# Kernel optimization log

Measured on AMD Instinct MI355X. Metric: run time of the kernel, lower is better.

## Reference

```python
import jax, jax.numpy as jnp
import numpy as np

B, L, D = 32, 4096, 1024


def setup_inputs() -> dict:
    key = jax.random.key(0)
    k_h, k_idx, k_w1, k_w2 = jax.random.split(key, 4)
    h = jax.random.normal(k_h, (B, L, D), dtype=jnp.float32)
    # 4 sorted positions per sample: [s1, e1, s2, e2]; +arange*2 guarantees
    # strict increase and a non-empty context region (s2 > e1 + 1).
    raw = jnp.sort(jax.random.randint(k_idx, (B, 4), 0, L - 10), axis=-1)
    pts = raw + jnp.arange(4, dtype=raw.dtype) * 2
    span1_idx = pts[:, 0:2].reshape(B, 1, 2).astype(jnp.int64)
    span2_idx = pts[:, 2:4].reshape(B, 1, 2).astype(jnp.int64)
    scale1 = 1.0 / np.sqrt(3 * D)
    scale2 = 1.0 / np.sqrt(D)
    W1 = jax.random.normal(k_w1, (3 * D, D), dtype=jnp.float32) * scale1
    b1 = jnp.zeros((D,), dtype=jnp.float32)
    W2 = jax.random.normal(k_w2, (D, D), dtype=jnp.float32) * scale2
    b2 = jnp.zeros((D,), dtype=jnp.float32)
    return {"h": h, "span1_idx": span1_idx, "span2_idx": span2_idx,
            "W1": W1, "b1": b1, "W2": W2, "b2": b2}


def _masked_mean(h, lo, hi_excl):
    # mean of h[b, lo[b]:hi_excl[b], :] over the length axis, vectorized
    pos = jnp.arange(h.shape[1])  # [L]
    mask = ((pos[None, :] >= lo[:, None]) & (pos[None, :] < hi_excl[:, None])).astype(h.dtype)  # [B,L]
    cnt = jnp.maximum(mask.sum(axis=1, keepdims=True), 1.0)  # [B,1]
    return jnp.einsum('bl,bld->bd', mask, h) / cnt  # [B,D]


def reference(h, span1_idx, span2_idx, W1, b1, W2, b2):
    s1, e1 = span1_idx[:, 0, 0], span1_idx[:, 0, 1]
    s2, e2 = span2_idx[:, 0, 0], span2_idx[:, 0, 1]
    span1_rep = _masked_mean(h, s1, e1 + 1)          # span tokens inclusive
    span2_rep = _masked_mean(h, s2, e2 + 1)
    context_rep = _masked_mean(h, e1 + 1, s2)        # tokens strictly between spans
    combined = jnp.concatenate([span1_rep, context_rep, span2_rep], axis=-1)  # [B,3D]
    hmid = jax.nn.relu(combined @ W1 + b1)
    out = hmid @ W2 + b2
    return out[:, None, :]  # [B,1,D]
```

## Files before the change

### kernel.cpp

```cpp
#include <hip/hip_runtime.h>

#define BB 32
#define LL 4096
#define DD 1024
#define G1 2048
#define K2_TILE 32
#define K3_TILE 16

static __device__ __forceinline__ int imax(int a, int b) { return a > b ? a : b; }
static __device__ __forceinline__ int imin(int a, int b) { return a < b ? a : b; }

__global__ __launch_bounds__(256) void k0_zero(float* __restrict__ sums_hmid,
                                               float* __restrict__ out) {
    const int i = blockIdx.x * 256 + threadIdx.x;
    const float4 z = make_float4(0.f, 0.f, 0.f, 0.f);
    if (i < 32768) ((float4*)sums_hmid)[i] = z;
    else ((float4*)out)[i - 32768] = z;
}

static __device__ __forceinline__ void accum_rows_add(const float* __restrict__ hb,
                                                      int beg, int end, float4& acc) {
    float4 a0 = make_float4(0.f, 0.f, 0.f, 0.f);
    float4 a1 = a0, a2 = a0, a3 = a0, a4 = a0, a5 = a0, a6 = a0, a7 = a0;
    int l = beg;
    for (; l + 8 <= end; l += 8) {
        float4 v0 = *(const float4*)(hb + (size_t)(l + 0) * DD);
        float4 v1 = *(const float4*)(hb + (size_t)(l + 1) * DD);
        float4 v2 = *(const float4*)(hb + (size_t)(l + 2) * DD);
        float4 v3 = *(const float4*)(hb + (size_t)(l + 3) * DD);
        float4 v4 = *(const float4*)(hb + (size_t)(l + 4) * DD);
        float4 v5 = *(const float4*)(hb + (size_t)(l + 5) * DD);
        float4 v6 = *(const float4*)(hb + (size_t)(l + 6) * DD);
        float4 v7 = *(const float4*)(hb + (size_t)(l + 7) * DD);
        a0.x += v0.x; a0.y += v0.y; a0.z += v0.z; a0.w += v0.w;
        a1.x += v1.x; a1.y += v1.y; a1.z += v1.z; a1.w += v1.w;
        a2.x += v2.x; a2.y += v2.y; a2.z += v2.z; a2.w += v2.w;
        a3.x += v3.x; a3.y += v3.y; a3.z += v3.z; a3.w += v3.w;
        a4.x += v4.x; a4.y += v4.y; a4.z += v4.z; a4.w += v4.w;
        a5.x += v5.x; a5.y += v5.y; a5.z += v5.z; a5.w += v5.w;
        a6.x += v6.x; a6.y += v6.y; a6.z += v6.z; a6.w += v6.w;
        a7.x += v7.x; a7.y += v7.y; a7.z += v7.z; a7.w += v7.w;
    }
    for (; l + 4 <= end; l += 4) {
        float4 v0 = *(const float4*)(hb + (size_t)(l + 0) * DD);
        float4 v1 = *(const float4*)(hb + (size_t)(l + 1) * DD);
        float4 v2 = *(const float4*)(hb + (size_t)(l + 2) * DD);
        float4 v3 = *(const float4*)(hb + (size_t)(l + 3) * DD);
        a0.x += v0.x; a0.y += v0.y; a0.z += v0.z; a0.w += v0.w;
        a1.x += v1.x; a1.y += v1.y; a1.z += v1.z; a1.w += v1.w;
        a2.x += v2.x; a2.y += v2.y; a2.z += v2.z; a2.w += v2.w;
        a3.x += v3.x; a3.y += v3.y; a3.z += v3.z; a3.w += v3.w;
    }
    for (; l < end; ++l) {
        float4 v = *(const float4*)(hb + (size_t)l * DD);
        a0.x += v.x; a0.y += v.y; a0.z += v.z; a0.w += v.w;
    }
    acc.x += ((a0.x + a1.x) + (a2.x + a3.x)) + ((a4.x + a5.x) + (a6.x + a7.x));
    acc.y += ((a0.y + a1.y) + (a2.y + a3.y)) + ((a4.y + a5.y) + (a6.y + a7.y));
    acc.z += ((a0.z + a1.z) + (a2.z + a3.z)) + ((a4.z + a5.z) + (a6.z + a7.z));
    acc.w += ((a0.w + a1.w) + (a2.w + a3.w)) + ((a4.w + a5.w) + (a6.w + a7.w));
}

__global__ __launch_bounds__(256) void k1_sums(const float* __restrict__ h,
                                               const int* __restrict__ sp1,
                                               const int* __restrict__ sp2,
                                               float* __restrict__ sums) {
    const int tid = threadIdx.x;

    int NC = 0;
#pragma unroll
    for (int b = 0; b < BB; ++b)
        NC += sp2[2 * b + 1] - sp1[2 * b] + 1;

    const int q = NC / G1, r = NC % G1;
    const int bk = blockIdx.x;
    int c0 = bk * q + imin(bk, r);
    const int c1 = c0 + q + (bk < r ? 1 : 0);
    if (c0 >= c1) return;

    int b = 0, base = 0, s1, e1, s2, e2, len;
    for (;; ++b) {
        s1 = sp1[2 * b]; e1 = sp1[2 * b + 1];
        s2 = sp2[2 * b]; e2 = sp2[2 * b + 1];
        len = e2 - s1 + 1;
        if (c0 < base + len) break;
        base += len;
    }

    for (;;) {
        const int cend = imin(c1, base + len);
        const int rb = s1 + (c0 - base);
        const int re = s1 + (cend - base);
        const float* hb = h + (size_t)b * LL * DD + (size_t)tid * 4;
        float* dstb = sums + (size_t)b * 3 * DD + (size_t)tid * 4;
        const int lo[3] = {rb, imax(rb, e1 + 1), imax(rb, s2)};
        const int hi[3] = {imin(re, e1 + 1), imin(re, s2), re};
#pragma unroll
        for (int s = 0; s < 3; ++s) {
            if (lo[s] < hi[s]) {
                float4 acc = make_float4(0.f, 0.f, 0.f, 0.f);
                accum_rows_add(hb, lo[s], hi[s], acc);
                float* d = dstb + s * DD;
                atomicAdd(d + 0, acc.x); atomicAdd(d + 1, acc.y);
                atomicAdd(d + 2, acc.z); atomicAdd(d + 3, acc.w);
            }
        }
        c0 = cend;
        if (c0 >= c1) break;
        base += len; ++b;
        s1 = sp1[2 * b]; e1 = sp1[2 * b + 1];
        s2 = sp2[2 * b]; e2 = sp2[2 * b + 1];
        len = e2 - s1 + 1;
    }
}

__global__ __launch_bounds__(256) void k2_gemm1(const float* __restrict__ sums,
                                                const int* __restrict__ sp1,
                                                const int* __restrict__ sp2,
                                                const float* __restrict__ W1,
                                                float* __restrict__ hmid) {
    __shared__ float cl[K2_TILE * BB];
    __shared__ float icl[BB];
    const int tid = threadIdx.x;
    const int j = blockIdx.x * 256 + tid;
    const int k0 = blockIdx.y * K2_TILE;
    const int seg = k0 / DD;

    if (tid < BB) {
        const int b = tid;
        const int s1 = sp1[2 * b], e1 = sp1[2 * b + 1];
        const int s2 = sp2[2 * b], e2 = sp2[2 * b + 1];
        const int cnt = (seg == 0) ? (e1 + 1 - s1) : (seg == 1) ? (s2 - e1 - 1) : (e2 + 1 - s2);
        icl[b] = 1.0f / (float)imax(cnt, 1);
    }
    __syncthreads();
    for (int i = tid; i < K2_TILE * BB; i += 256) {
        const int kk = i / BB;
        const int b = i % BB;
        cl[i] = sums[(size_t)b * (3 * DD) + (k0 + kk)] * icl[b];
    }
    __syncthreads();

    float acc[BB];
#pragma unroll
    for (int b = 0; b < BB; ++b) acc[b] = 0.f;

    const float* w = W1 + (size_t)k0 * DD + j;
#pragma unroll 8
    for (int kk = 0; kk < K2_TILE; ++kk) {
        const float wv = w[(size_t)kk * DD];
        const float4* c4 = (const float4*)(cl + kk * BB);
#pragma unroll
        for (int qq = 0; qq < BB / 4; ++qq) {
            float4 c = c4[qq];
            acc[4 * qq + 0] = fmaf(c.x, wv, acc[4 * qq + 0]);
            acc[4 * qq + 1] = fmaf(c.y, wv, acc[4 * qq + 1]);
            acc[4 * qq + 2] = fmaf(c.z, wv, acc[4 * qq + 2]);
            acc[4 * qq + 3] = fmaf(c.w, wv, acc[4 * qq + 3]);
        }
    }
#pragma unroll
    for (int b = 0; b < BB; ++b) atomicAdd(&hmid[(size_t)b * DD + j], acc[b]);
}

__global__ __launch_bounds__(256) void k3_gemm2(const float* __restrict__ hmid,
                                                const float* __restrict__ b1,
                                                const float* __restrict__ W2,
                                                const float* __restrict__ b2,
                                                float* __restrict__ out) {
    __shared__ float al[K3_TILE * BB];
    const int tid = threadIdx.x;
    const int j = blockIdx.x * 256 + tid;
    const int k0 = blockIdx.y * K3_TILE;

    for (int i = tid; i < K3_TILE * BB; i += 256) {
        const int kk = i / BB;
        const int b = i % BB;
        const float v = hmid[(size_t)b * DD + (k0 + kk)] + b1[k0 + kk];
        al[i] = fmaxf(v, 0.f);
    }
    __syncthreads();

    float acc[BB];
    const float bias = (blockIdx.y == 0) ? b2[j] : 0.f;
#pragma unroll
    for (int b = 0; b < BB; ++b) acc[b] = bias;

    const float* w = W2 + (size_t)k0 * DD + j;
#pragma unroll 8
    for (int kk = 0; kk < K3_TILE; ++kk) {
        const float wv = w[(size_t)kk * DD];
        const float4* c4 = (const float4*)(al + kk * BB);
#pragma unroll
        for (int qq = 0; qq < BB / 4; ++qq) {
            float4 c = c4[qq];
            acc[4 * qq + 0] = fmaf(c.x, wv, acc[4 * qq + 0]);
            acc[4 * qq + 1] = fmaf(c.y, wv, acc[4 * qq + 1]);
            acc[4 * qq + 2] = fmaf(c.z, wv, acc[4 * qq + 2]);
            acc[4 * qq + 3] = fmaf(c.w, wv, acc[4 * qq + 3]);
        }
    }
#pragma unroll
    for (int b = 0; b < BB; ++b) atomicAdd(&out[(size_t)b * DD + j], acc[b]);
}

extern "C" void kernel_launch(void* const* d_in, const int* in_sizes, int n_in,
                              void* d_out, int out_size, void* d_ws, size_t ws_size,
                              hipStream_t stream) {
    const float* h = (const float*)d_in[0];
    const int* sp1 = (const int*)d_in[1];
    const int* sp2 = (const int*)d_in[2];
    const float* W1 = (const float*)d_in[3];
    const float* b1 = (const float*)d_in[4];
    const float* W2 = (const float*)d_in[5];
    const float* b2 = (const float*)d_in[6];
    float* out = (float*)d_out;

    float* sums = (float*)d_ws;
    float* hmid = sums + BB * 3 * DD;

    k0_zero<<<160, 256, 0, stream>>>((float*)d_ws, out);
    k1_sums<<<G1, 256, 0, stream>>>(h, sp1, sp2, sums);
    k2_gemm1<<<dim3(DD / 256, 3 * DD / K2_TILE), 256, 0, stream>>>(sums, sp1, sp2, W1, hmid);
    k3_gemm2<<<dim3(DD / 256, DD / K3_TILE), 256, 0, stream>>>(hmid, b1, W2, b2, out);
}
```

Before: 111.9 us.

## Fuse span-sum and two GEMM kernels into one persistent kernel with grid barriers

The three separate launches (span sums, first GEMM, second GEMM) become one persistent kernel of 768 blocks. Phases are separated by software grid barriers built on atomic counters and flags in the workspace, and the zero kernel now also clears those barrier words. The goal is to drop launch gaps and tail effects between stages. In exchange the span-sum phase has fewer blocks (768 vs 2048) with a shallower unroll, and the barriers rely on every block being co-resident, which risks a deadlock if occupancy falls short.

```diff
diff --git a/kernel.cpp b/kernel.cpp
--- a/kernel.cpp
+++ b/kernel.cpp
@@ -3,44 +3,46 @@
 #define BB 32
 #define LL 4096
 #define DD 1024
-#define G1 2048
-#define K2_TILE 32
-#define K3_TILE 16
+#define GRID 768
+#define K2T 32
+#define K3T 16
 
 static __device__ __forceinline__ int imax(int a, int b) { return a > b ? a : b; }
 static __device__ __forceinline__ int imin(int a, int b) { return a < b ? a : b; }
 
-__global__ __launch_bounds__(256) void k0_zero(float* __restrict__ sums_hmid,
+#define BAR_OFF 131072
+
+__global__ __launch_bounds__(256) void k0_zero(float* __restrict__ ws,
                                                float* __restrict__ out) {
     const int i = blockIdx.x * 256 + threadIdx.x;
     const float4 z = make_float4(0.f, 0.f, 0.f, 0.f);
-    if (i < 32768) ((float4*)sums_hmid)[i] = z;
-    else ((float4*)out)[i - 32768] = z;
+    if (i < 32832) ((float4*)ws)[i] = z;
+    else if (i < 32832 + 8192) ((float4*)out)[i - 32832] = z;
+}
+
+static __device__ __forceinline__ void gbar(unsigned* cnt, unsigned* flag, int nb) {
+    __syncthreads();
+    if (threadIdx.x == 0) {
+        __threadfence();
+        const unsigned old = __hip_atomic_fetch_add(cnt, 1u, __ATOMIC_ACQ_REL,
+                                                    __HIP_MEMORY_SCOPE_AGENT);
+        if ((int)old == nb - 1) {
+            __hip_atomic_store(flag, 1u, __ATOMIC_RELEASE, __HIP_MEMORY_SCOPE_AGENT);
+        } else {
+            while (__hip_atomic_load(flag, __ATOMIC_ACQUIRE,
+                                     __HIP_MEMORY_SCOPE_AGENT) == 0u)
+                __builtin_amdgcn_s_sleep(1);
+        }
+        __threadfence();
+    }
+    __syncthreads();
 }
 
 static __device__ __forceinline__ void accum_rows_add(const float* __restrict__ hb,
                                                       int beg, int end, float4& acc) {
     float4 a0 = make_float4(0.f, 0.f, 0.f, 0.f);
-    float4 a1 = a0, a2 = a0, a3 = a0, a4 = a0, a5 = a0, a6 = a0, a7 = a0;
+    float4 a1 = a0, a2 = a0, a3 = a0;
     int l = beg;
-    for (; l + 8 <= end; l += 8) {
-        float4 v0 = *(const float4*)(hb + (size_t)(l + 0) * DD);
-        float4 v1 = *(const float4*)(hb + (size_t)(l + 1) * DD);
-        float4 v2 = *(const float4*)(hb + (size_t)(l + 2) * DD);
-        float4 v3 = *(const float4*)(hb + (size_t)(l + 3) * DD);
-        float4 v4 = *(const float4*)(hb + (size_t)(l + 4) * DD);
-        float4 v5 = *(const float4*)(hb + (size_t)(l + 5) * DD);
-        float4 v6 = *(const float4*)(hb + (size_t)(l + 6) * DD);
-        float4 v7 = *(const float4*)(hb + (size_t)(l + 7) * DD);
-        a0.x += v0.x; a0.y += v0.y; a0.z += v0.z; a0.w += v0.w;
-        a1.x += v1.x; a1.y += v1.y; a1.z += v1.z; a1.w += v1.w;
-        a2.x += v2.x; a2.y += v2.y; a2.z += v2.z; a2.w += v2.w;
-        a3.x += v3.x; a3.y += v3.y; a3.z += v3.z; a3.w += v3.w;
-        a4.x += v4.x; a4.y += v4.y; a4.z += v4.z; a4.w += v4.w;
-        a5.x += v5.x; a5.y += v5.y; a5.z += v5.z; a5.w += v5.w;
-        a6.x += v6.x; a6.y += v6.y; a6.z += v6.z; a6.w += v6.w;
-        a7.x += v7.x; a7.y += v7.y; a7.z += v7.z; a7.w += v7.w;
-    }
     for (; l + 4 <= end; l += 4) {
         float4 v0 = *(const float4*)(hb + (size_t)(l + 0) * DD);
         float4 v1 = *(const float4*)(hb + (size_t)(l + 1) * DD);
@@ -55,153 +57,159 @@
         float4 v = *(const float4*)(hb + (size_t)l * DD);
         a0.x += v.x; a0.y += v.y; a0.z += v.z; a0.w += v.w;
     }
-    acc.x += ((a0.x + a1.x) + (a2.x + a3.x)) + ((a4.x + a5.x) + (a6.x + a7.x));
-    acc.y += ((a0.y + a1.y) + (a2.y + a3.y)) + ((a4.y + a5.y) + (a6.y + a7.y));
-    acc.z += ((a0.z + a1.z) + (a2.z + a3.z)) + ((a4.z + a5.z) + (a6.z + a7.z));
-    acc.w += ((a0.w + a1.w) + (a2.w + a3.w)) + ((a4.w + a5.w) + (a6.w + a7.w));
-}
-
-__global__ __launch_bounds__(256) void k1_sums(const float* __restrict__ h,
-                                               const int* __restrict__ sp1,
-                                               const int* __restrict__ sp2,
-                                               float* __restrict__ sums) {
-    const int tid = threadIdx.x;
-
-    int NC = 0;
-#pragma unroll
-    for (int b = 0; b < BB; ++b)
-        NC += sp2[2 * b + 1] - sp1[2 * b] + 1;
-
-    const int q = NC / G1, r = NC % G1;
-    const int bk = blockIdx.x;
-    int c0 = bk * q + imin(bk, r);
-    const int c1 = c0 + q + (bk < r ? 1 : 0);
-    if (c0 >= c1) return;
-
-    int b = 0, base = 0, s1, e1, s2, e2, len;
-    for (;; ++b) {
-        s1 = sp1[2 * b]; e1 = sp1[2 * b + 1];
-        s2 = sp2[2 * b]; e2 = sp2[2 * b + 1];
-        len = e2 - s1 + 1;
-        if (c0 < base + len) break;
-        base += len;
-    }
-
-    for (;;) {
-        const int cend = imin(c1, base + len);
-        const int rb = s1 + (c0 - base);
-        const int re = s1 + (cend - base);
-        const float* hb = h + (size_t)b * LL * DD + (size_t)tid * 4;
-        float* dstb = sums + (size_t)b * 3 * DD + (size_t)tid * 4;
-        const int lo[3] = {rb, imax(rb, e1 + 1), imax(rb, s2)};
-        const int hi[3] = {imin(re, e1 + 1), imin(re, s2), re};
-#pragma unroll
-        for (int s = 0; s < 3; ++s) {
-            if (lo[s] < hi[s]) {
-                float4 acc = make_float4(0.f, 0.f, 0.f, 0.f);
-                accum_rows_add(hb, lo[s], hi[s], acc);
-                float* d = dstb + s * DD;
-                atomicAdd(d + 0, acc.x); atomicAdd(d + 1, acc.y);
-                atomicAdd(d + 2, acc.z); atomicAdd(d + 3, acc.w);
-            }
-        }
-        c0 = cend;
-        if (c0 >= c1) break;
-        base += len; ++b;
-        s1 = sp1[2 * b]; e1 = sp1[2 * b + 1];
-        s2 = sp2[2 * b]; e2 = sp2[2 * b + 1];
-        len = e2 - s1 + 1;
-    }
-}
-
-__global__ __launch_bounds__(256) void k2_gemm1(const float* __restrict__ sums,
+    acc.x += (a0.x + a1.x) + (a2.x + a3.x);
+    acc.y += (a0.y + a1.y) + (a2.y + a3.y);
+    acc.z += (a0.z + a1.z) + (a2.z + a3.z);
+    acc.w += (a0.w + a1.w) + (a2.w + a3.w);
+}
+
+__global__ __launch_bounds__(256, 3) void fused(const float* __restrict__ h,
                                                 const int* __restrict__ sp1,
                                                 const int* __restrict__ sp2,
                                                 const float* __restrict__ W1,
-                                                float* __restrict__ hmid) {
-    __shared__ float cl[K2_TILE * BB];
-    __shared__ float icl[BB];
-    const int tid = threadIdx.x;
-    const int j = blockIdx.x * 256 + tid;
-    const int k0 = blockIdx.y * K2_TILE;
-    const int seg = k0 / DD;
-
-    if (tid < BB) {
-        const int b = tid;
-        const int s1 = sp1[2 * b], e1 = sp1[2 * b + 1];
-        const int s2 = sp2[2 * b], e2 = sp2[2 * b + 1];
-        const int cnt = (seg == 0) ? (e1 + 1 - s1) : (seg == 1) ? (s2 - e1 - 1) : (e2 + 1 - s2);
-        icl[b] = 1.0f / (float)imax(cnt, 1);
-    }
-    __syncthreads();
-    for (int i = tid; i < K2_TILE * BB; i += 256) {
-        const int kk = i / BB;
-        const int b = i % BB;
-        cl[i] = sums[(size_t)b * (3 * DD) + (k0 + kk)] * icl[b];
-    }
-    __syncthreads();
-
-    float acc[BB];
-#pragma unroll
-    for (int b = 0; b < BB; ++b) acc[b] = 0.f;
-
-    const float* w = W1 + (size_t)k0 * DD + j;
-#pragma unroll 8
-    for (int kk = 0; kk < K2_TILE; ++kk) {
-        const float wv = w[(size_t)kk * DD];
-        const float4* c4 = (const float4*)(cl + kk * BB);
-#pragma unroll
-        for (int qq = 0; qq < BB / 4; ++qq) {
-            float4 c = c4[qq];
-            acc[4 * qq + 0] = fmaf(c.x, wv, acc[4 * qq + 0]);
-            acc[4 * qq + 1] = fmaf(c.y, wv, acc[4 * qq + 1]);
-            acc[4 * qq + 2] = fmaf(c.z, wv, acc[4 * qq + 2]);
-            acc[4 * qq + 3] = fmaf(c.w, wv, acc[4 * qq + 3]);
-        }
-    }
-#pragma unroll
-    for (int b = 0; b < BB; ++b) atomicAdd(&hmid[(size_t)b * DD + j], acc[b]);
-}
-
-__global__ __launch_bounds__(256) void k3_gemm2(const float* __restrict__ hmid,
                                                 const float* __restrict__ b1,
                                                 const float* __restrict__ W2,
                                                 const float* __restrict__ b2,
-                                                float* __restrict__ out) {
-    __shared__ float al[K3_TILE * BB];
+                                                float* __restrict__ sums,
+                                                float* __restrict__ hmid,
+                                                float* __restrict__ out,
+                                                unsigned* __restrict__ bar) {
     const int tid = threadIdx.x;
-    const int j = blockIdx.x * 256 + tid;
-    const int k0 = blockIdx.y * K3_TILE;
-
-    for (int i = tid; i < K3_TILE * BB; i += 256) {
-        const int kk = i / BB;
-        const int b = i % BB;
-        const float v = hmid[(size_t)b * DD + (k0 + kk)] + b1[k0 + kk];
-        al[i] = fmaxf(v, 0.f);
-    }
-    __syncthreads();
-
-    float acc[BB];
-    const float bias = (blockIdx.y == 0) ? b2[j] : 0.f;
-#pragma unroll
-    for (int b = 0; b < BB; ++b) acc[b] = bias;
-
-    const float* w = W2 + (size_t)k0 * DD + j;
+    const int bk = blockIdx.x;
+
+    __shared__ float lds[K2T * BB];
+    __shared__ float icl[BB];
+
+    {
+        int NC = 0;
+#pragma unroll
+        for (int b = 0; b < BB; ++b)
+            NC += sp2[2 * b + 1] - sp1[2 * b] + 1;
+
+        const int q = NC / GRID, r = NC % GRID;
+        int c0 = bk * q + imin(bk, r);
+        const int c1 = c0 + q + (bk < r ? 1 : 0);
+        if (c0 < c1) {
+            int b = 0, base = 0, s1, e1, s2, e2, len;
+            for (;; ++b) {
+                s1 = sp1[2 * b]; e1 = sp1[2 * b + 1];
+                s2 = sp2[2 * b]; e2 = sp2[2 * b + 1];
+                len = e2 - s1 + 1;
+                if (c0 < base + len) break;
+                base += len;
+            }
+            for (;;) {
+                const int cend = imin(c1, base + len);
+                const int rb = s1 + (c0 - base);
+                const int re = s1 + (cend - base);
+                const float* hb = h + (size_t)b * LL * DD + (size_t)tid * 4;
+                float* dstb = sums + (size_t)b * 3 * DD + (size_t)tid * 4;
+                const int lo[3] = {rb, imax(rb, e1 + 1), imax(rb, s2)};
+                const int hi[3] = {imin(re, e1 + 1), imin(re, s2), re};
+#pragma unroll
+                for (int s = 0; s < 3; ++s) {
+                    if (lo[s] < hi[s]) {
+                        float4 acc = make_float4(0.f, 0.f, 0.f, 0.f);
+                        accum_rows_add(hb, lo[s], hi[s], acc);
+                        float* d = dstb + s * DD;
+                        atomicAdd(d + 0, acc.x); atomicAdd(d + 1, acc.y);
+                        atomicAdd(d + 2, acc.z); atomicAdd(d + 3, acc.w);
+                    }
+                }
+                c0 = cend;
+                if (c0 >= c1) break;
+                base += len; ++b;
+                s1 = sp1[2 * b]; e1 = sp1[2 * b + 1];
+                s2 = sp2[2 * b]; e2 = sp2[2 * b + 1];
+                len = e2 - s1 + 1;
+            }
+        }
+    }
+    gbar(&bar[0], &bar[16], GRID);
+
+    if (bk < 384) {
+        const int jc = bk & 3;
+        const int j = jc * 256 + tid;
+        const int kt2 = bk >> 2;
+        const int k0 = kt2 * K2T;
+        const int seg = k0 / DD;
+        if (tid < BB) {
+            const int b = tid;
+            const int s1 = sp1[2 * b], e1 = sp1[2 * b + 1];
+            const int s2 = sp2[2 * b], e2 = sp2[2 * b + 1];
+            const int cnt = (seg == 0) ? (e1 + 1 - s1) : (seg == 1) ? (s2 - e1 - 1)
+                                                                    : (e2 + 1 - s2);
+            icl[b] = 1.0f / (float)imax(cnt, 1);
+        }
+        __syncthreads();
+        for (int i = tid; i < K2T * BB; i += 256) {
+            const int kk = i >> 5;
+            const int b = i & 31;
+            const float v = __hip_atomic_load(&sums[(size_t)b * (3 * DD) + (k0 + kk)],
+                                              __ATOMIC_RELAXED, __HIP_MEMORY_SCOPE_AGENT);
+            lds[i] = v * icl[b];
+        }
+        __syncthreads();
+
+        float acc[BB];
+#pragma unroll
+        for (int b = 0; b < BB; ++b) acc[b] = 0.f;
+
+        const float* w = W1 + (size_t)k0 * DD + j;
 #pragma unroll 8
-    for (int kk = 0; kk < K3_TILE; ++kk) {
-        const float wv = w[(size_t)kk * DD];
-        const float4* c4 = (const float4*)(al + kk * BB);
-#pragma unroll
-        for (int qq = 0; qq < BB / 4; ++qq) {
-            float4 c = c4[qq];
-            acc[4 * qq + 0] = fmaf(c.x, wv, acc[4 * qq + 0]);
-            acc[4 * qq + 1] = fmaf(c.y, wv, acc[4 * qq + 1]);
-            acc[4 * qq + 2] = fmaf(c.z, wv, acc[4 * qq + 2]);
-            acc[4 * qq + 3] = fmaf(c.w, wv, acc[4 * qq + 3]);
-        }
-    }
-#pragma unroll
-    for (int b = 0; b < BB; ++b) atomicAdd(&out[(size_t)b * DD + j], acc[b]);
+        for (int kk = 0; kk < K2T; ++kk) {
+            const float wv = w[(size_t)kk * DD];
+            const float4* c4 = (const float4*)(lds + kk * BB);
+#pragma unroll
+            for (int qq = 0; qq < BB / 4; ++qq) {
+                float4 c = c4[qq];
+                acc[4 * qq + 0] = fmaf(c.x, wv, acc[4 * qq + 0]);
+                acc[4 * qq + 1] = fmaf(c.y, wv, acc[4 * qq + 1]);
+                acc[4 * qq + 2] = fmaf(c.z, wv, acc[4 * qq + 2]);
+                acc[4 * qq + 3] = fmaf(c.w, wv, acc[4 * qq + 3]);
+            }
+        }
+#pragma unroll
+        for (int b = 0; b < BB; ++b) atomicAdd(&hmid[(size_t)b * DD + j], acc[b]);
+    }
+    gbar(&bar[32], &bar[48], GRID);
+
+    if (bk < 256) {
+        const int jc = bk & 3;
+        const int j = jc * 256 + tid;
+        const int kt3 = bk >> 2;
+        const int k0 = kt3 * K3T;
+        for (int i = tid; i < K3T * BB; i += 256) {
+            const int kk = i >> 5;
+            const int b = i & 31;
+            const float v = __hip_atomic_load(&hmid[(size_t)b * DD + (k0 + kk)],
+                                              __ATOMIC_RELAXED, __HIP_MEMORY_SCOPE_AGENT);
+            lds[i] = fmaxf(v + b1[k0 + kk], 0.f);
+        }
+        __syncthreads();
+
+        float acc[BB];
+        const float bias = (kt3 == 0) ? b2[j] : 0.f;
+#pragma unroll
+        for (int b = 0; b < BB; ++b) acc[b] = bias;
+
+        const float* w = W2 + (size_t)k0 * DD + j;
+#pragma unroll 8
+        for (int kk = 0; kk < K3T; ++kk) {
+            const float wv = w[(size_t)kk * DD];
+            const float4* c4 = (const float4*)(lds + kk * BB);
+#pragma unroll
+            for (int qq = 0; qq < BB / 4; ++qq) {
+                float4 c = c4[qq];
+                acc[4 * qq + 0] = fmaf(c.x, wv, acc[4 * qq + 0]);
+                acc[4 * qq + 1] = fmaf(c.y, wv, acc[4 * qq + 1]);
+                acc[4 * qq + 2] = fmaf(c.z, wv, acc[4 * qq + 2]);
+                acc[4 * qq + 3] = fmaf(c.w, wv, acc[4 * qq + 3]);
+            }
+        }
+#pragma unroll
+        for (int b = 0; b < BB; ++b) atomicAdd(&out[(size_t)b * DD + j], acc[b]);
+    }
 }
 
 extern "C" void kernel_launch(void* const* d_in, const int* in_sizes, int n_in,
@@ -216,11 +224,12 @@
     const float* b2 = (const float*)d_in[6];
     float* out = (float*)d_out;
 
-    float* sums = (float*)d_ws;
-    float* hmid = sums + BB * 3 * DD;
-
-    k0_zero<<<160, 256, 0, stream>>>((float*)d_ws, out);
-    k1_sums<<<G1, 256, 0, stream>>>(h, sp1, sp2, sums);
-    k2_gemm1<<<dim3(DD / 256, 3 * DD / K2_TILE), 256, 0, stream>>>(sums, sp1, sp2, W1, hmid);
-    k3_gemm2<<<dim3(DD / 256, DD / K3_TILE), 256, 0, stream>>>(hmid, b1, W2, b2, out);
-}
+    float* ws = (float*)d_ws;
+    float* sums = ws;
+    float* hmid = ws + BB * 3 * DD;
+    unsigned* bar = (unsigned*)(ws + BAR_OFF);
+
+    k0_zero<<<161, 256, 0, stream>>>(ws, out);
+    fused<<<GRID, 256, 0, stream>>>(h, sp1, sp2, W1, b1, W2, b2,
+                                    sums, hmid, out, bar);
+}
```

After: 360.1 us. 3.22x slower.
